# Optimization experiments

Hardware: AMD Instinct MI355X
Metric: run time of the kernel (lower is better)

## Reference

```python
import jax, jax.numpy as jnp
import numpy as np

N = 2048      # oscillators
K = 8         # neighbors per oscillator (connectivity0)
B = 32        # batch
T = 20        # time_steps
EPS0 = 1.0    # update_rate
ANNEAL = 0.0  # anneal


def setup_inputs() -> dict:
    key = jax.random.key(0)
    k1, k2, k3 = jax.random.split(key, 3)
    coupling = jax.random.normal(k1, (B, N, K), dtype=jnp.float32)
    connectivity = jax.random.randint(k2, (N, K), 0, N)
    phase0 = 2.0 * jnp.pi * jax.random.uniform(k3, (B, N), dtype=jnp.float32)
    omega = jnp.zeros((B, N), dtype=jnp.float32)
    return {"coupling": coupling, "phase0": phase0, "omega": omega,
            "connectivity": connectivity}


def reference(coupling, phase0, omega, connectivity):
    # Scatter sparse per-neighbor couplings [B,N,K] into dense [B,N,N]
    # (torch scatter_ dim=2 with the same index per batch element).
    rows = jnp.arange(N)[:, None]                      # [N,1]
    C = jnp.zeros((B, N, N), coupling.dtype).at[:, rows, connectivity].set(coupling)
    # n = number of nonzero couplings per row  [B,N]
    n = jnp.abs(jnp.sign(C)).sum(axis=2)

    def step(carry, i):
        phase, eps = carry                             # phase [B,N]
        s, c = jnp.sin(phase), jnp.cos(phase)
        Cs = jnp.einsum('bnm,bm->bn', C, s)
        Cc = jnp.einsum('bnm,bm->bn', C, c)
        delta = eps * (Cs * c - Cc * s) / n
        phase_new = phase + delta + omega
        # eps_anneal called after each update with step index i
        eps_new = eps - ANNEAL * i.astype(eps.dtype) * eps / T
        return (phase_new, eps_new), phase_new

    (_, _), phases = jax.lax.scan(step, (phase0, jnp.float32(EPS0)), jnp.arange(T))
    # phase_list: initial phase followed by T updated phases  [T+1,B,N]
    return jnp.concatenate([phase0[None], phases], axis=0)
```

## Files before the change

kernel.cpp:

```cpp
#include <hip/hip_runtime.h>

#define NN 2048
#define KK 8
#define BB 32
#define TT 20

__global__ __launch_bounds__(1024) void osci_kernel(
    const float* __restrict__ coupling,
    const float* __restrict__ phase0,
    const float* __restrict__ omega,
    const int*   __restrict__ conn,
    float*       __restrict__ out)
{
    const int b   = blockIdx.x;
    const int tid = threadIdx.x;
    const int i0  = tid * 2;

    __shared__ float ph_buf[2][NN];

    int   cidx[2][KK];
    float w[2][KK];
    float om[2];
    float ph[2];

    {
        const float2 p  = ((const float2*)(phase0 + (size_t)b * NN))[tid];
        const float2 o  = ((const float2*)(omega  + (size_t)b * NN))[tid];
        ph[0] = p.x; ph[1] = p.y;
        om[0] = o.x; om[1] = o.y;
        ((float2*)(out + (size_t)b * NN))[tid] = p;
        *(float2*)&ph_buf[0][i0] = p;

        #pragma unroll
        for (int t = 0; t < 2; ++t) {
            const int i = i0 + t;
            const int4   ja = ((const int4*)(conn + (size_t)i * KK))[0];
            const int4   jb = ((const int4*)(conn + (size_t)i * KK))[1];
            const float4 va = ((const float4*)(coupling + ((size_t)b * NN + i) * KK))[0];
            const float4 vb = ((const float4*)(coupling + ((size_t)b * NN + i) * KK))[1];
            int   jj[KK] = {ja.x, ja.y, ja.z, ja.w, jb.x, jb.y, jb.z, jb.w};
            float vv[KK] = {va.x, va.y, va.z, va.w, vb.x, vb.y, vb.z, vb.w};

            int cnt = 0;
            #pragma unroll
            for (int k = 0; k < KK; ++k) {
                bool over = false;
                #pragma unroll
                for (int k2 = k + 1; k2 < KK; ++k2) over = over || (jj[k2] == jj[k]);
                if (over) vv[k] = 0.0f;
                if (vv[k] != 0.0f) ++cnt;
            }
            const float nf = (float)cnt;
            #pragma unroll
            for (int k = 0; k < KK; ++k) {
                cidx[t][k] = jj[k];
                w[t][k]    = vv[k] / nf;
            }
        }
    }
    __syncthreads();

    for (int step = 0; step < TT; ++step) {
        const int cur = step & 1;
        const int nxt = cur ^ 1;

        const float ri0 = ph[0], ri1 = ph[1];
        float acc0 = 0.0f, acc1 = 0.0f;
        #pragma unroll
        for (int k = 0; k < KK; ++k) {
            const float pj0 = ph_buf[cur][cidx[0][k]];
            const float pj1 = ph_buf[cur][cidx[1][k]];
            acc0 += w[0][k] * __sinf(pj0 - ri0);
            acc1 += w[1][k] * __sinf(pj1 - ri1);
        }
        const float pn0 = ri0 + acc0 + om[0];
        const float pn1 = ri1 + acc1 + om[1];
        ph[0] = pn0; ph[1] = pn1;

        *(float2*)&ph_buf[nxt][i0] = make_float2(pn0, pn1);
        *(float2*)&out[((size_t)(step + 1) * BB + b) * NN + i0] = make_float2(pn0, pn1);

        __syncthreads();
    }
}

extern "C" void kernel_launch(void* const* d_in, const int* in_sizes, int n_in,
                              void* d_out, int out_size, void* d_ws, size_t ws_size,
                              hipStream_t stream) {
    const float* coupling = (const float*)d_in[0];
    const float* phase0   = (const float*)d_in[1];
    const float* omega    = (const float*)d_in[2];
    const int*   conn     = (const int*)d_in[3];
    float* out = (float*)d_out;

    osci_kernel<<<BB, 1024, 0, stream>>>(coupling, phase0, omega, conn, out);
}
```

Before: 83.96 us.

## Reorder neighbor gathers per wave to spread LDS bank accesses

Adds a one-time setup pass in which each wave counts, through shared-memory atomics, how many of its lanes target each LDS bank. Each lane then permutes its 8 neighbor indices and weights so that lanes sharing a bank are spread across different k-iterations. The goal is fewer bank conflicts in the random ph_buf gathers done over the 20 timesteps. The cost is the atomics, the permutation logic and extra registers during setup. The reordering only changes summation order, so results can differ slightly in floating point.

```diff
diff --git a/kernel.cpp b/kernel.cpp
--- a/kernel.cpp
+++ b/kernel.cpp
@@ -14,18 +14,19 @@
 {
     const int b   = blockIdx.x;
     const int tid = threadIdx.x;
+    const int wv  = tid >> 6;
     const int i0  = tid * 2;
 
-    __shared__ float ph_buf[2][NN];
+    __shared__ float    ph_buf[2][NN];
+    __shared__ unsigned cnt[2][16][32];
 
-    int   cidx[2][KK];
-    float w[2][KK];
-    float om[2];
-    float ph[2];
+    float ph[2], om[2];
+    int   jj[2][KK];
+    float vv[2][KK];
 
     {
-        const float2 p  = ((const float2*)(phase0 + (size_t)b * NN))[tid];
-        const float2 o  = ((const float2*)(omega  + (size_t)b * NN))[tid];
+        const float2 p = ((const float2*)(phase0 + (size_t)b * NN))[tid];
+        const float2 o = ((const float2*)(omega  + (size_t)b * NN))[tid];
         ph[0] = p.x; ph[1] = p.y;
         om[0] = o.x; om[1] = o.y;
         ((float2*)(out + (size_t)b * NN))[tid] = p;
@@ -38,24 +39,54 @@
             const int4   jb = ((const int4*)(conn + (size_t)i * KK))[1];
             const float4 va = ((const float4*)(coupling + ((size_t)b * NN + i) * KK))[0];
             const float4 vb = ((const float4*)(coupling + ((size_t)b * NN + i) * KK))[1];
-            int   jj[KK] = {ja.x, ja.y, ja.z, ja.w, jb.x, jb.y, jb.z, jb.w};
-            float vv[KK] = {va.x, va.y, va.z, va.w, vb.x, vb.y, vb.z, vb.w};
+            int   jx[KK] = {ja.x, ja.y, ja.z, ja.w, jb.x, jb.y, jb.z, jb.w};
+            float vx[KK] = {va.x, va.y, va.z, va.w, vb.x, vb.y, vb.z, vb.w};
 
-            int cnt = 0;
+            int cnt_nz = 0;
             #pragma unroll
             for (int k = 0; k < KK; ++k) {
                 bool over = false;
                 #pragma unroll
-                for (int k2 = k + 1; k2 < KK; ++k2) over = over || (jj[k2] == jj[k]);
-                if (over) vv[k] = 0.0f;
-                if (vv[k] != 0.0f) ++cnt;
+                for (int k2 = k + 1; k2 < KK; ++k2) over = over || (jx[k2] == jx[k]);
+                if (over) vx[k] = 0.0f;
+                if (vx[k] != 0.0f) ++cnt_nz;
             }
-            const float nf = (float)cnt;
+            const float nf = (float)cnt_nz;
             #pragma unroll
-            for (int k = 0; k < KK; ++k) {
-                cidx[t][k] = jj[k];
-                w[t][k]    = vv[k] / nf;
+            for (int k = 0; k < KK; ++k) { jj[t][k] = jx[k]; vv[t][k] = vx[k] / nf; }
+        }
+    }
+
+    ((unsigned*)cnt)[tid] = 0u;
+    __syncthreads();
+
+    int   jS[2][KK];
+    float wS[2][KK];
+    #pragma unroll
+    for (int g = 0; g < 2; ++g) {
+        unsigned slotpack = 0u;
+        unsigned free_m   = 0xFFu;
+        #pragma unroll
+        for (int m = 0; m < KK; ++m) {
+            const unsigned bank = (unsigned)jj[g][m] & 31u;
+            const unsigned r    = atomicAdd(&cnt[g][wv][bank], 1u);
+            const unsigned p    = r & 7u;
+            const unsigned rot  = ((free_m >> p) | (free_m << (8u - p))) & 0xFFu;
+            const unsigned d    = (unsigned)__ffs((int)rot) - 1u;
+            const unsigned s    = (p + d) & 7u;
+            free_m &= ~(1u << s);
+            slotpack |= s << (m * 4);
+        }
+        #pragma unroll
+        for (int s = 0; s < KK; ++s) {
+            int jv = 0; float wvv = 0.0f;
+            #pragma unroll
+            for (int m = 0; m < KK; ++m) {
+                const bool hit = (((slotpack >> (m * 4)) & 7u) == (unsigned)s);
+                jv  = hit ? jj[g][m] : jv;
+                wvv = hit ? vv[g][m] : wvv;
             }
+            jS[g][s] = jv; wS[g][s] = wvv;
         }
     }
     __syncthreads();
@@ -68,10 +99,10 @@
         float acc0 = 0.0f, acc1 = 0.0f;
         #pragma unroll
         for (int k = 0; k < KK; ++k) {
-            const float pj0 = ph_buf[cur][cidx[0][k]];
-            const float pj1 = ph_buf[cur][cidx[1][k]];
-            acc0 += w[0][k] * __sinf(pj0 - ri0);
-            acc1 += w[1][k] * __sinf(pj1 - ri1);
+            const float pj0 = ph_buf[cur][jS[0][k]];
+            const float pj1 = ph_buf[cur][jS[1][k]];
+            acc0 += wS[0][k] * __sinf(pj0 - ri0);
+            acc1 += wS[1][k] * __sinf(pj1 - ri1);
         }
         const float pn0 = ri0 + acc0 + om[0];
         const float pn1 = ri1 + acc1 + om[1];
```

Result: slower. 87.73 us (+4.5%).
